# Optimization experiments

Measured on AMD Instinct MI355X. Metric: run time of the kernel, lower is better.

Reference implementation:

```python
import jax, jax.numpy as jnp
import numpy as np

B, S, D, K = 128, 200, 128, 4
NQ, NC = 10000, 500


def setup_inputs() -> dict:
    key = jax.random.key(0)
    ks = jax.random.split(key, 20)
    f = jnp.float32
    inp = {}
    inp["question_seq"] = jax.random.randint(ks[0], (B, S), 0, NQ)
    inp["hint_attempt_seq"] = jax.random.randint(ks[1], (B, S), 0, 12)
    inp["correct_seq"] = jax.random.randint(ks[2], (B, S), 0, 2)
    inp["interval_time_seq"] = jax.random.randint(ks[3], (B, S), 0, 100)
    inp["use_time_seq"] = jax.random.randint(ks[4], (B, S), 0, 100)
    inp["q2c_table"] = jax.random.randint(ks[5], (NQ, K), 0, NC)
    inp["q2c_mask_table"] = jax.random.randint(ks[6], (NQ, K), 0, 2)
    s = 0.1
    inp["embed_question"] = jax.random.normal(ks[7], (NQ, D), f) * s
    inp["embed_question_disc"] = jax.random.normal(ks[8], (NQ, 1), f) * s
    inp["embed_concept"] = jax.random.normal(ks[9], (NC, D), f) * s
    inp["embed_interval_time"] = jax.random.normal(ks[10], (100, D), f) * s
    inp["embed_use_time"] = jax.random.normal(ks[11], (100, D), f) * s
    inp["embed_hint_attempt"] = jax.random.normal(ks[12], (12, D), f) * s
    inp["W_fuse"] = jax.random.normal(ks[13], (2 * D, D), f) / np.float32(np.sqrt(2 * D))
    inp["b_fuse"] = jnp.zeros((D,), f)
    inp["W_absorb"] = jax.random.normal(ks[14], (3 * D, D), f) / np.float32(np.sqrt(3 * D))
    inp["b_absorb"] = jnp.zeros((D,), f)
    inp["W_forget"] = jax.random.normal(ks[15], (3 * D, D), f) / np.float32(np.sqrt(3 * D))
    inp["b_forget"] = jnp.zeros((D,), f)
    inp["latent0"] = jax.random.normal(ks[16], (B, D), f) * 0.1  # xavier-init latent_pre
    return inp


def _cos(a, b, eps=1e-8):
    # torch.cosine_similarity semantics with eps clamp on each norm
    num = jnp.sum(a * b, axis=-1)
    na = jnp.sqrt(jnp.sum(a * a, axis=-1))
    nb = jnp.sqrt(jnp.sum(b * b, axis=-1))
    return num / (jnp.maximum(na, eps) * jnp.maximum(nb, eps))


def _forward(question_seq, hint_attempt_seq, correct_seq, interval_time_seq, use_time_seq,
             q2c_table, q2c_mask_table,
             embed_question, embed_question_disc, embed_concept, embed_interval_time,
             embed_use_time, embed_hint_attempt,
             W_fuse, b_fuse, W_absorb, b_absorb, W_forget, b_forget, latent0):
    f = latent0.dtype
    qe = embed_question[question_seq]                                # [B,S,D]
    qd = jax.nn.sigmoid(embed_question_disc[question_seq]) * 10.0    # [B,S,1]
    ce = jnp.broadcast_to(correct_seq.astype(f)[:, :, None], qe.shape)  # [B,S,D]
    ite = embed_interval_time[interval_time_seq]                     # [B,S,D]
    ute = embed_use_time[use_time_seq]                               # [B,S,D]
    hae = embed_hint_attempt[hint_attempt_seq]                       # [B,S,D]
    cp = embed_concept[q2c_table[question_seq]]                      # [B,S,K,D]
    m = q2c_mask_table[question_seq].astype(f)                       # [B,S,K]

    tm = lambda x: jnp.swapaxes(x, 0, 1)  # time-major for scan
    xs = (tm(qe[:, :-1]), tm(ce[:, :-1]), tm(ute[:, :-1]), tm(hae[:, :-1]), tm(ite[:, :-1]),
          tm(cp[:, :-1]), tm(cp[:, 1:]), tm(qd[:, 1:]), tm(m[:, :-1]))

    def step(lp, x):
        qe_t, ce_t, ute_t, hae_t, ite_t, cp_t, cp_t1, qd_t1, m_t = x
        inter = jnp.concatenate([qe_t, ce_t], axis=-1) @ W_fuse + b_fuse
        absorb = jnp.concatenate([inter, ute_t, hae_t], axis=-1) @ W_absorb + b_absorb
        forget = jax.nn.sigmoid(jnp.concatenate([lp, ite_t, inter], axis=-1) @ W_forget + b_forget)
        lc = lp * forget + absorb  # dropout p=0 -> identity
        qdiff = (_cos(qe_t[:, None, :], cp_t) + 1.0) * 0.5   # [B,K]
        uab = (_cos(lc[:, None, :], cp_t1) + 1.0) * 0.5      # [B,K]
        logit = qd_t1[:, 0] * jnp.sum((uab - qdiff) * m_t, axis=-1)  # [B]
        return lc, jax.nn.sigmoid(logit)

    _, ys = jax.lax.scan(step, latent0, xs)  # ys: [S-1, B]
    y = jnp.concatenate([ys.T, jnp.zeros((latent0.shape[0], 1), f)], axis=1)  # [B,S], last col 0
    return y


def reference(question_seq, hint_attempt_seq, correct_seq, interval_time_seq, use_time_seq,
              q2c_table, q2c_mask_table,
              embed_question, embed_question_disc, embed_concept, embed_interval_time,
              embed_use_time, embed_hint_attempt,
              W_fuse, b_fuse, W_absorb, b_absorb, W_forget, b_forget, latent0):
    return _forward(question_seq, hint_attempt_seq, correct_seq, interval_time_seq, use_time_seq,
                    q2c_table, q2c_mask_table,
                    embed_question, embed_question_disc, embed_concept, embed_interval_time,
                    embed_use_time, embed_hint_attempt,
                    W_fuse, b_fuse, W_absorb, b_absorb, W_forget, b_forget, latent0)
```

## Files before the change

### kernel.cpp

```cpp
#include <hip/hip_runtime.h>
#include <hip/hip_bf16.h>

typedef unsigned short u16;

#define Bb  128
#define Ss  200
#define Tt  199
#define Dd  128
#define Kk  4
#define NQq 10000
#define NCc 500
#define CHK 16
#define NCH 13

__device__ inline float bf2f(u16 u) {
    union { unsigned int i; float f; } x;
    x.i = ((unsigned int)u) << 16;
    return x.f;
}

__device__ inline float ldf(const void* p, int i, int m) {
    if (m) return ((const float*)p)[i];
    return bf2f(((const u16*)p)[i]);
}

__device__ inline void stf(void* p, int i, int m, float v) {
    if (m) ((float*)p)[i] = v;
    else ((__hip_bfloat16*)p)[i] = __float2bfloat16(v);
}

__device__ inline int clampi(int v, int lo, int hi) {
    return v < lo ? lo : (v > hi ? hi : v);
}

__device__ inline float wave_red(float v) {
#pragma unroll
    for (int m = 32; m >= 1; m >>= 1) v += __shfl_xor(v, m);
    return v;
}

__device__ inline float4 f4add(float4 a, float4 b) {
    return make_float4(a.x + b.x, a.y + b.y, a.z + b.z, a.w + b.w);
}
__device__ inline float4 f4fma(float s, float4 a, float4 b) {
    return make_float4(fmaf(s, a.x, b.x), fmaf(s, a.y, b.y),
                       fmaf(s, a.z, b.z), fmaf(s, a.w, b.w));
}

__device__ inline int detect_mode(const void* Eq) {
    const u16* q = (const u16*)Eq;
    const int l = threadIdx.x & 63;
    float mx = 0.f;
#pragma unroll
    for (int k = 0; k < 4; ++k) {
        float a = fabsf(bf2f(q[l * 4 + k]));
        if (!(a == a)) a = 3.0e38f;
        mx = fmaxf(mx, a);
    }
#pragma unroll
    for (int s = 32; s >= 1; s >>= 1) mx = fmaxf(mx, __shfl_xor(mx, s));
    return (mx > 1.0e6f) ? 1 : 0;
}

__global__ __launch_bounds__(128) void k_prep(
    const void* Eq, const void* Wf, const void* Wa, const void* Wg,
    const void* bfu, const void* ba, const void* bg,
    const void* Eut, const void* Eha, const void* Eit, const void* Ec,
    float* cnorm, float* BabT, float* BfgT,
    float* vA0, float* vA1, float* vF0, float* vF1,
    float* PA_ut, float* PA_ha, float* PF_it) {
    const int m = detect_mode(Eq);
    const int bi = blockIdx.x, tid = threadIdx.x;
    __shared__ float cs2s[128];
    __shared__ float tmp[2];
    if (bi < 500) {
        const int c = bi;
        float v = ldf(Ec, c * 128 + tid, m);
        float s = wave_red(v * v);
        if ((tid & 63) == 0) tmp[tid >> 6] = s;
        __syncthreads();
        if (tid == 0) cnorm[c] = fmaxf(sqrtf(tmp[0] + tmp[1]), 1e-8f);
    } else if (bi < 628) {
        const int r = bi - 500;
        float acc = 0.f;
        for (int j = 0; j < 128; ++j)
            acc += ldf(Wf, r * 128 + j, m) * ldf(Wa, j * 128 + tid, m);
        BabT[r * 128 + tid] = acc;
    } else if (bi < 756) {
        const int r = bi - 628;
        float acc = 0.f;
        for (int j = 0; j < 128; ++j)
            acc += ldf(Wf, r * 128 + j, m) * ldf(Wg, (256 + j) * 128 + tid, m);
        BfgT[r * 128 + tid] = acc;
    } else if (bi == 756) {
        float s = 0.f;
        for (int r = 0; r < 128; ++r) s += ldf(Wf, (128 + r) * 128 + tid, m);
        cs2s[tid] = s;
        __syncthreads();
        float a0 = 0.f, a1 = 0.f;
        for (int j = 0; j < 128; ++j) {
            float wv = ldf(Wa, j * 128 + tid, m);
            a0 += ldf(bfu, j, m) * wv;
            a1 += cs2s[j] * wv;
        }
        vA0[tid] = a0 + ldf(ba, tid, m);
        vA1[tid] = a1;
    } else if (bi == 757) {
        float s = 0.f;
        for (int r = 0; r < 128; ++r) s += ldf(Wf, (128 + r) * 128 + tid, m);
        cs2s[tid] = s;
        __syncthreads();
        float a0 = 0.f, a1 = 0.f;
        for (int j = 0; j < 128; ++j) {
            float wv = ldf(Wg, (256 + j) * 128 + tid, m);
            a0 += ldf(bfu, j, m) * wv;
            a1 += cs2s[j] * wv;
        }
        vF0[tid] = a0 + ldf(bg, tid, m);
        vF1[tid] = a1;
    } else if (bi < 858) {
        const int r = bi - 758;
        float acc = 0.f;
        for (int j = 0; j < 128; ++j)
            acc += ldf(Eut, r * 128 + j, m) * ldf(Wa, (128 + j) * 128 + tid, m);
        PA_ut[r * 128 + tid] = acc;
    } else if (bi < 870) {
        const int r = bi - 858;
        float acc = 0.f;
        for (int j = 0; j < 128; ++j)
            acc += ldf(Eha, r * 128 + j, m) * ldf(Wa, (256 + j) * 128 + tid, m);
        PA_ha[r * 128 + tid] = acc;
    } else {
        const int r = bi - 870;
        float acc = 0.f;
        for (int j = 0; j < 128; ++j)
            acc += ldf(Eit, r * 128 + j, m) * ldf(Wg, (128 + j) * 128 + tid, m);
        PF_it[r * 128 + tid] = acc;
    }
}

__global__ __launch_bounds__(256) void k_mid(
    const void* Eq, const void* Eqd, const void* Ec,
    const int* q2c, const int* q2cm,
    const float* BabT, const float* BfgT, const float* cnorm,
    float* PA_q, float* PF_q, float* qdm, float* qd10) {
    const int m = detect_mode(Eq);
    const int tid = threadIdx.x;
    const int bi = blockIdx.x;
    if (bi < 313) {
        __shared__ float At[32][36];
        __shared__ float Bt0[32][128];
        __shared__ float Bt1[32][128];
        const int r0 = bi * 32;
        float acc0[2][8], acc1[2][8];
#pragma unroll
        for (int j = 0; j < 2; ++j)
#pragma unroll
            for (int i = 0; i < 8; ++i) { acc0[j][i] = 0.f; acc1[j][i] = 0.f; }
        const int tx = tid & 15, ty = tid >> 4;
        for (int ks = 0; ks < 4; ++ks) {
            {
                const int row = tid >> 3, seg = tid & 7;
                const int q = clampi(r0 + row, 0, NQq - 1);
                const int ei = q * 128 + ks * 32 + seg * 4;
                float* dst = &At[row][seg * 4];
                if (m) {
                    float4 v = *(const float4*)((const float*)Eq + ei);
                    dst[0] = v.x; dst[1] = v.y; dst[2] = v.z; dst[3] = v.w;
                } else {
                    uint2 v = *(const uint2*)((const u16*)Eq + ei);
                    dst[0] = bf2f((u16)(v.x & 0xffff)); dst[1] = bf2f((u16)(v.x >> 16));
                    dst[2] = bf2f((u16)(v.y & 0xffff)); dst[3] = bf2f((u16)(v.y >> 16));
                }
            }
            {
                const float4* s0 = (const float4*)(BabT + ks * 32 * 128);
                const float4* s1 = (const float4*)(BfgT + ks * 32 * 128);
                float4* d0 = (float4*)&Bt0[0][0];
                float4* d1 = (float4*)&Bt1[0][0];
#pragma unroll
                for (int k = 0; k < 4; ++k) {
                    d0[tid + k * 256] = s0[tid + k * 256];
                    d1[tid + k * 256] = s1[tid + k * 256];
                }
            }
            __syncthreads();
#pragma unroll
            for (int kk = 0; kk < 32; kk += 4) {
                float a_[2][4];
                *(float4*)&a_[0][0] = *(const float4*)&At[ty * 2 + 0][kk];
                *(float4*)&a_[1][0] = *(const float4*)&At[ty * 2 + 1][kk];
#pragma unroll
                for (int q = 0; q < 4; ++q) {
                    float4 b0 = *(const float4*)&Bt0[kk + q][tx * 8];
                    float4 b1 = *(const float4*)&Bt0[kk + q][tx * 8 + 4];
                    float4 c0 = *(const float4*)&Bt1[kk + q][tx * 8];
                    float4 c1 = *(const float4*)&Bt1[kk + q][tx * 8 + 4];
#pragma unroll
                    for (int j = 0; j < 2; ++j) {
                        const float av = a_[j][q];
                        acc0[j][0] += av * b0.x; acc0[j][1] += av * b0.y;
                        acc0[j][2] += av * b0.z; acc0[j][3] += av * b0.w;
                        acc0[j][4] += av * b1.x; acc0[j][5] += av * b1.y;
                        acc0[j][6] += av * b1.z; acc0[j][7] += av * b1.w;
                        acc1[j][0] += av * c0.x; acc1[j][1] += av * c0.y;
                        acc1[j][2] += av * c0.z; acc1[j][3] += av * c0.w;
                        acc1[j][4] += av * c1.x; acc1[j][5] += av * c1.y;
                        acc1[j][6] += av * c1.z; acc1[j][7] += av * c1.w;
                    }
                }
            }
            __syncthreads();
        }
#pragma unroll
        for (int j = 0; j < 2; ++j) {
            const int q = r0 + ty * 2 + j;
            if (q < NQq) {
                float* oa = PA_q + q * 128 + tx * 8;
                float* of = PF_q + q * 128 + tx * 8;
#pragma unroll
                for (int i = 0; i < 8; ++i) { oa[i] = acc0[j][i]; of[i] = acc1[j][i]; }
            }
        }
    } else {
        const int wv = tid >> 6, lane = tid & 63;
        const int q = (bi - 313) * 4 + wv;
        const float qa = ldf(Eq, q * 128 + lane, m);
        const float qb = ldf(Eq, q * 128 + 64 + lane, m);
        const float nqc = fmaxf(sqrtf(wave_red(qa * qa + qb * qb)), 1e-8f);
        const int4 cc = ((const int4*)q2c)[q];
        const int4 mm = ((const int4*)q2cm)[q];
        const int cks[4] = {clampi(cc.x, 0, NCc - 1), clampi(cc.y, 0, NCc - 1),
                            clampi(cc.z, 0, NCc - 1), clampi(cc.w, 0, NCc - 1)};
        const int ms[4]  = {mm.x, mm.y, mm.z, mm.w};
        float qs = 0.f;
#pragma unroll
        for (int k = 0; k < 4; ++k) {
            const int ck = cks[k];
            float dot = wave_red(qa * ldf(Ec, ck * 128 + lane, m) +
                                 qb * ldf(Ec, ck * 128 + 64 + lane, m));
            qs += (float)ms[k] * (0.5f * dot / (nqc * cnorm[ck]) + 0.5f);
        }
        if (lane == 0) {
            qdm[q] = qs;
            qd10[q] = 10.f / (1.f + __expf(-ldf(Eqd, q, m)));
        }
    }
}

__global__ __launch_bounds__(256) void p4_scan(
    const int* q_seq, const int* ut_seq, const int* ha_seq, const int* it_seq,
    const int* c_seq,
    const void* Eq, const void* Wg, const void* L0,
    const float* PA_q, const float* PA_ut, const float* PA_ha,
    const float* PF_q, const float* PF_it,
    const float* vA0, const float* vA1, const float* vF0, const float* vF1,
    float* lc_seq) {
    const int m = detect_mode(Eq);
    const int b = blockIdx.x;
    const int tid = threadIdx.x;
    const int wv = tid >> 6, l = tid & 63;
    const int d0 = 2 * l;
    const int ib = wv << 5;
    const int dd = ib + (l & 31);

    __shared__ float part[2][4][128];
    __shared__ float st_ab[CHK * 128];
    __shared__ float st_pf[CHK * 128];

    float wA[32], wB[32];
#pragma unroll
    for (int k = 0; k < 32; ++k) {
        wA[k] = ldf(Wg, (ib + k) * 128 + d0, m);
        wB[k] = ldf(Wg, (ib + k) * 128 + d0 + 1, m);
    }
    float lc = (l < 32) ? ldf(L0, b * 128 + dd, m) : 0.f;

    const int srow = tid >> 4, seg = tid & 15;
    const int off8 = seg * 8;
    const float4 A0a = *(const float4*)(vA0 + off8), A0b = *(const float4*)(vA0 + off8 + 4);
    const float4 A1a = *(const float4*)(vA1 + off8), A1b = *(const float4*)(vA1 + off8 + 4);
    const float4 F0a = *(const float4*)(vF0 + off8), F0b = *(const float4*)(vF0 + off8 + 4);
    const float4 F1a = *(const float4*)(vF1 + off8), F1b = *(const float4*)(vF1 + off8 + 4);

    float4 qa0, qa1, ua0, ua1, ga0, ga1, qf0, qf1, if0, if1;
    float cf;
#define LOAD_CHUNK(C)                                                          \
    {                                                                          \
        int tt = (C) * CHK + srow; if (tt > Tt - 1) tt = Tt - 1;               \
        const int base = b * Ss + tt;                                          \
        const int qt = clampi(q_seq[base], 0, NQq - 1);                        \
        const int ut = clampi(ut_seq[base], 0, 99);                            \
        const int ha = clampi(ha_seq[base], 0, 11);                            \
        const int it = clampi(it_seq[base], 0, 99);                            \
        cf = (float)c_seq[base];                                               \
        const float* pq = PA_q + qt * 128 + off8;                              \
        qa0 = *(const float4*)pq; qa1 = *(const float4*)(pq + 4);              \
        const float* pu = PA_ut + ut * 128 + off8;                             \
        ua0 = *(const float4*)pu; ua1 = *(const float4*)(pu + 4);              \
        const float* ph = PA_ha + ha * 128 + off8;                             \
        ga0 = *(const float4*)ph; ga1 = *(const float4*)(ph + 4);              \
        const float* pf = PF_q + qt * 128 + off8;                              \
        qf0 = *(const float4*)pf; qf1 = *(const float4*)(pf + 4);              \
        const float* pi = PF_it + it * 128 + off8;                             \
        if0 = *(const float4*)pi; if1 = *(const float4*)(pi + 4);              \
    }

    LOAD_CHUNK(0)
    float lcbuf[CHK];
    int par = 0;

    for (int c = 0; c < NCH; ++c) {
        __syncthreads();
        {
            float4 ab0 = f4fma(cf, A1a, f4add(f4add(qa0, ua0), f4add(ga0, A0a)));
            float4 ab1 = f4fma(cf, A1b, f4add(f4add(qa1, ua1), f4add(ga1, A0b)));
            float4 pf0 = f4fma(cf, F1a, f4add(qf0, f4add(if0, F0a)));
            float4 pf1 = f4fma(cf, F1b, f4add(qf1, f4add(if1, F0b)));
            float4* sa = (float4*)(st_ab + srow * 128 + off8);
            sa[0] = ab0; sa[1] = ab1;
            float4* sp = (float4*)(st_pf + srow * 128 + off8);
            sp[0] = pf0; sp[1] = pf1;
        }
        if (c + 1 < NCH) LOAD_CHUNK(c + 1)
        __syncthreads();

#pragma unroll
        for (int s = 0; s < CHK; ++s) {
            float pa = 0.f, pb = 0.f;
#pragma unroll
            for (int k = 0; k < 32; ++k) {
                const float u = __uint_as_float(
                    __builtin_amdgcn_readlane(__float_as_uint(lc), k));
                pa = fmaf(u, wA[k], pa);
                pb = fmaf(u, wB[k], pb);
            }
            *(float2*)&part[par][wv][d0] = make_float2(pa, pb);
            __syncthreads();
            if (l < 32) {
                const float fs = part[par][0][dd] + part[par][1][dd]
                               + part[par][2][dd] + part[par][3][dd];
                const float ab = st_ab[(s << 7) + dd];
                const float pf = st_pf[(s << 7) + dd];
                const float fg = 1.f / (1.f + __expf(-(fs + pf)));
                lc = lc * fg + ab;
                lcbuf[s] = lc;
            }
            par ^= 1;
        }
        if (l < 32) {
#pragma unroll
            for (int s = 0; s < CHK; ++s) {
                const int t = c * CHK + s;
                if (t < Tt)
                    lc_seq[((long)t * 128 + b) * 128 + dd] = lcbuf[s];
            }
        }
    }
#undef LOAD_CHUNK
}

__global__ __launch_bounds__(256) void p5_out(
    const int* q_seq, const int* q2c, const int* q2cm,
    const float* lc_seq, const float* qdm, const float* qd10,
    const float* cnorm, const void* Eq, const void* Ec, void* out) {
    const int m = detect_mode(Eq);
    const int wv = threadIdx.x >> 6, lane = threadIdx.x & 63;
    const int r = blockIdx.x * 4 + wv;
    const int t = r >> 7, b = r & 127;
    const int qt  = clampi(q_seq[b * Ss + t], 0, NQq - 1);
    const int qt1 = clampi(q_seq[b * Ss + t + 1], 0, NQq - 1);
    const int4 mm = ((const int4*)q2cm)[qt];
    int4 ci = ((const int4*)q2c)[qt1];
    const int c0 = clampi(ci.x, 0, NCc - 1), c1 = clampi(ci.y, 0, NCc - 1);
    const int c2 = clampi(ci.z, 0, NCc - 1), c3 = clampi(ci.w, 0, NCc - 1);
    const float la = lc_seq[(long)r * 128 + lane];
    const float lb = lc_seq[(long)r * 128 + 64 + lane];
    float nl = la * la + lb * lb;
    float d0 = la * ldf(Ec, c0 * 128 + lane, m) + lb * ldf(Ec, c0 * 128 + 64 + lane, m);
    float d1 = la * ldf(Ec, c1 * 128 + lane, m) + lb * ldf(Ec, c1 * 128 + 64 + lane, m);
    float d2 = la * ldf(Ec, c2 * 128 + lane, m) + lb * ldf(Ec, c2 * 128 + 64 + lane, m);
    float d3 = la * ldf(Ec, c3 * 128 + lane, m) + lb * ldf(Ec, c3 * 128 + 64 + lane, m);
#pragma unroll
    for (int s = 32; s >= 1; s >>= 1) {
        nl += __shfl_xor(nl, s);
        d0 += __shfl_xor(d0, s); d1 += __shfl_xor(d1, s);
        d2 += __shfl_xor(d2, s); d3 += __shfl_xor(d3, s);
    }
    if (lane == 0) {
        const float inl = 1.f / fmaxf(sqrtf(nl), 1e-8f);
        const float accv = (float)mm.x * (0.5f * d0 * inl / cnorm[c0] + 0.5f)
                         + (float)mm.y * (0.5f * d1 * inl / cnorm[c1] + 0.5f)
                         + (float)mm.z * (0.5f * d2 * inl / cnorm[c2] + 0.5f)
                         + (float)mm.w * (0.5f * d3 * inl / cnorm[c3] + 0.5f);
        const float logit = qd10[qt1] * (accv - qdm[qt]);
        stf(out, b * Ss + t, m, 1.f / (1.f + __expf(-logit)));
        if (t == 0) stf(out, b * Ss + 199, m, 0.f);
    }
}

extern "C" void kernel_launch(void* const* d_in, const int* in_sizes, int n_in,
                              void* d_out, int out_size, void* d_ws, size_t ws_size,
                              hipStream_t stream) {
    (void)in_sizes; (void)n_in; (void)out_size; (void)ws_size;
    const int* q_seq  = (const int*)d_in[0];
    const int* ha_seq = (const int*)d_in[1];
    const int* c_seq  = (const int*)d_in[2];
    const int* it_seq = (const int*)d_in[3];
    const int* ut_seq = (const int*)d_in[4];
    const int* q2c    = (const int*)d_in[5];
    const int* q2cm   = (const int*)d_in[6];
    const void* Eq   = d_in[7];
    const void* Eqd  = d_in[8];
    const void* Ec   = d_in[9];
    const void* Eit  = d_in[10];
    const void* Eut  = d_in[11];
    const void* Eha  = d_in[12];
    const void* Wf   = d_in[13];
    const void* bfu  = d_in[14];
    const void* Wa   = d_in[15];
    const void* ba   = d_in[16];
    const void* Wg   = d_in[17];
    const void* bg   = d_in[18];
    const void* L0   = d_in[19];

    float* cnorm = (float*)d_ws;
    float* vA0   = cnorm + 512;
    float* vA1   = vA0 + 128;
    float* vF0   = vA1 + 128;
    float* vF1   = vF0 + 128;
    float* BabT  = vF1 + 128;
    float* BfgT  = BabT + 16384;
    float* PA_ut = BfgT + 16384;
    float* PA_ha = PA_ut + 12800;
    float* PF_it = PA_ha + 1536;
    float* qdm   = PF_it + 12800;
    float* qd10  = qdm + 10016;
    float* PA_q  = qd10 + 10016;
    float* PF_q  = PA_q + 1280000;
    float* lc_seq= PF_q + 1280000;

    hipLaunchKernelGGL(k_prep, dim3(970), dim3(128), 0, stream,
                       Eq, Wf, Wa, Wg, bfu, ba, bg, Eut, Eha, Eit, Ec,
                       cnorm, BabT, BfgT, vA0, vA1, vF0, vF1, PA_ut, PA_ha, PF_it);
    hipLaunchKernelGGL(k_mid, dim3(2813), dim3(256), 0, stream,
                       Eq, Eqd, Ec, q2c, q2cm, BabT, BfgT, cnorm,
                       PA_q, PF_q, qdm, qd10);
    hipLaunchKernelGGL(p4_scan, dim3(Bb), dim3(256), 0, stream,
                       q_seq, ut_seq, ha_seq, it_seq, c_seq, Eq, Wg, L0,
                       PA_q, PA_ut, PA_ha, PF_q, PF_it,
                       vA0, vA1, vF0, vF1, lc_seq);
    hipLaunchKernelGGL(p5_out, dim3(Tt * Bb / 4), dim3(256), 0, stream,
                       q_seq, q2c, q2cm, lc_seq, qdm, qd10, cnorm, Eq, Ec, d_out);
}
```

Before: 235.4 us.

## Restructure prep kernels, inline concept norms, and overlap chunk loads in scan

Moves the question-difficulty work out of the GEMM kernel into k_prep, packs paired matmul rows into 256-thread blocks, and splits the PA_q/PF_q GEMM into its own kernel. Concept norms are now recomputed inline with a wave reduction instead of coming from a precomputed cnorm table, which removes that dependency. In the scan, the next chunk's prefetch is moved to step 1 so it overlaps compute. The absorb and forget values are preloaded into registers, and the readlane dot products use two accumulators to shorten the dependency chain. The cost is extra shuffle reductions for the norms in p5_out and the qdm jobs.

```diff
diff --git a/kernel.cpp b/kernel.cpp
--- a/kernel.cpp
+++ b/kernel.cpp
@@ -6,8 +6,6 @@
 #define Bb  128
 #define Ss  200
 #define Tt  199
-#define Dd  128
-#define Kk  4
 #define NQq 10000
 #define NCc 500
 #define CHK 16
@@ -62,169 +60,78 @@
     return (mx > 1.0e6f) ? 1 : 0;
 }
 
-__global__ __launch_bounds__(128) void k_prep(
-    const void* Eq, const void* Wf, const void* Wa, const void* Wg,
+__global__ __launch_bounds__(256) void k_prep(
+    const void* Eq, const void* Eqd, const void* Wf, const void* Wa, const void* Wg,
     const void* bfu, const void* ba, const void* bg,
     const void* Eut, const void* Eha, const void* Eit, const void* Ec,
-    float* cnorm, float* BabT, float* BfgT,
+    const int* q2c, const int* q2cm,
+    float* BabT, float* BfgT,
     float* vA0, float* vA1, float* vF0, float* vF1,
-    float* PA_ut, float* PA_ha, float* PF_it) {
+    float* PA_ut, float* PA_ha, float* PF_it, float* qdm, float* qd10) {
     const int m = detect_mode(Eq);
-    const int bi = blockIdx.x, tid = threadIdx.x;
+    const int job = blockIdx.x, tid = threadIdx.x;
     __shared__ float cs2s[128];
-    __shared__ float tmp[2];
-    if (bi < 500) {
-        const int c = bi;
-        float v = ldf(Ec, c * 128 + tid, m);
-        float s = wave_red(v * v);
-        if ((tid & 63) == 0) tmp[tid >> 6] = s;
-        __syncthreads();
-        if (tid == 0) cnorm[c] = fmaxf(sqrtf(tmp[0] + tmp[1]), 1e-8f);
-    } else if (bi < 628) {
-        const int r = bi - 500;
+    if (job < 128) {
+        const int r = job, col = tid & 127;
         float acc = 0.f;
-        for (int j = 0; j < 128; ++j)
-            acc += ldf(Wf, r * 128 + j, m) * ldf(Wa, j * 128 + tid, m);
-        BabT[r * 128 + tid] = acc;
-    } else if (bi < 756) {
-        const int r = bi - 628;
-        float acc = 0.f;
-        for (int j = 0; j < 128; ++j)
-            acc += ldf(Wf, r * 128 + j, m) * ldf(Wg, (256 + j) * 128 + tid, m);
-        BfgT[r * 128 + tid] = acc;
-    } else if (bi == 756) {
-        float s = 0.f;
-        for (int r = 0; r < 128; ++r) s += ldf(Wf, (128 + r) * 128 + tid, m);
-        cs2s[tid] = s;
+        if (tid < 128) {
+            for (int j = 0; j < 128; ++j)
+                acc += ldf(Wf, r * 128 + j, m) * ldf(Wa, j * 128 + col, m);
+            BabT[r * 128 + col] = acc;
+        } else {
+            for (int j = 0; j < 128; ++j)
+                acc += ldf(Wf, r * 128 + j, m) * ldf(Wg, (256 + j) * 128 + col, m);
+            BfgT[r * 128 + col] = acc;
+        }
+    } else if (job == 128) {
+        const int col = tid & 127;
+        if (tid < 128) {
+            float s = 0.f;
+            for (int r2 = 0; r2 < 128; ++r2) s += ldf(Wf, (128 + r2) * 128 + col, m);
+            cs2s[col] = s;
+        }
         __syncthreads();
         float a0 = 0.f, a1 = 0.f;
-        for (int j = 0; j < 128; ++j) {
-            float wv = ldf(Wa, j * 128 + tid, m);
-            a0 += ldf(bfu, j, m) * wv;
-            a1 += cs2s[j] * wv;
-        }
-        vA0[tid] = a0 + ldf(ba, tid, m);
-        vA1[tid] = a1;
-    } else if (bi == 757) {
-        float s = 0.f;
-        for (int r = 0; r < 128; ++r) s += ldf(Wf, (128 + r) * 128 + tid, m);
-        cs2s[tid] = s;
-        __syncthreads();
-        float a0 = 0.f, a1 = 0.f;
-        for (int j = 0; j < 128; ++j) {
-            float wv = ldf(Wg, (256 + j) * 128 + tid, m);
-            a0 += ldf(bfu, j, m) * wv;
-            a1 += cs2s[j] * wv;
-        }
-        vF0[tid] = a0 + ldf(bg, tid, m);
-        vF1[tid] = a1;
-    } else if (bi < 858) {
-        const int r = bi - 758;
+        if (tid < 128) {
+            for (int j = 0; j < 128; ++j) {
+                const float wv = ldf(Wa, j * 128 + col, m);
+                a0 += ldf(bfu, j, m) * wv;
+                a1 += cs2s[j] * wv;
+            }
+            vA0[col] = a0 + ldf(ba, col, m);
+            vA1[col] = a1;
+        } else {
+            for (int j = 0; j < 128; ++j) {
+                const float wv = ldf(Wg, (256 + j) * 128 + col, m);
+                a0 += ldf(bfu, j, m) * wv;
+                a1 += cs2s[j] * wv;
+            }
+            vF0[col] = a0 + ldf(bg, col, m);
+            vF1[col] = a1;
+        }
+    } else if (job < 229) {
+        const int r = job - 129, col = tid & 127;
         float acc = 0.f;
-        for (int j = 0; j < 128; ++j)
-            acc += ldf(Eut, r * 128 + j, m) * ldf(Wa, (128 + j) * 128 + tid, m);
-        PA_ut[r * 128 + tid] = acc;
-    } else if (bi < 870) {
-        const int r = bi - 858;
-        float acc = 0.f;
-        for (int j = 0; j < 128; ++j)
-            acc += ldf(Eha, r * 128 + j, m) * ldf(Wa, (256 + j) * 128 + tid, m);
-        PA_ha[r * 128 + tid] = acc;
-    } else {
-        const int r = bi - 870;
-        float acc = 0.f;
-        for (int j = 0; j < 128; ++j)
-            acc += ldf(Eit, r * 128 + j, m) * ldf(Wg, (128 + j) * 128 + tid, m);
-        PF_it[r * 128 + tid] = acc;
-    }
-}
-
-__global__ __launch_bounds__(256) void k_mid(
-    const void* Eq, const void* Eqd, const void* Ec,
-    const int* q2c, const int* q2cm,
-    const float* BabT, const float* BfgT, const float* cnorm,
-    float* PA_q, float* PF_q, float* qdm, float* qd10) {
-    const int m = detect_mode(Eq);
-    const int tid = threadIdx.x;
-    const int bi = blockIdx.x;
-    if (bi < 313) {
-        __shared__ float At[32][36];
-        __shared__ float Bt0[32][128];
-        __shared__ float Bt1[32][128];
-        const int r0 = bi * 32;
-        float acc0[2][8], acc1[2][8];
-#pragma unroll
-        for (int j = 0; j < 2; ++j)
-#pragma unroll
-            for (int i = 0; i < 8; ++i) { acc0[j][i] = 0.f; acc1[j][i] = 0.f; }
-        const int tx = tid & 15, ty = tid >> 4;
-        for (int ks = 0; ks < 4; ++ks) {
-            {
-                const int row = tid >> 3, seg = tid & 7;
-                const int q = clampi(r0 + row, 0, NQq - 1);
-                const int ei = q * 128 + ks * 32 + seg * 4;
-                float* dst = &At[row][seg * 4];
-                if (m) {
-                    float4 v = *(const float4*)((const float*)Eq + ei);
-                    dst[0] = v.x; dst[1] = v.y; dst[2] = v.z; dst[3] = v.w;
-                } else {
-                    uint2 v = *(const uint2*)((const u16*)Eq + ei);
-                    dst[0] = bf2f((u16)(v.x & 0xffff)); dst[1] = bf2f((u16)(v.x >> 16));
-                    dst[2] = bf2f((u16)(v.y & 0xffff)); dst[3] = bf2f((u16)(v.y >> 16));
-                }
-            }
-            {
-                const float4* s0 = (const float4*)(BabT + ks * 32 * 128);
-                const float4* s1 = (const float4*)(BfgT + ks * 32 * 128);
-                float4* d0 = (float4*)&Bt0[0][0];
-                float4* d1 = (float4*)&Bt1[0][0];
-#pragma unroll
-                for (int k = 0; k < 4; ++k) {
-                    d0[tid + k * 256] = s0[tid + k * 256];
-                    d1[tid + k * 256] = s1[tid + k * 256];
-                }
-            }
-            __syncthreads();
-#pragma unroll
-            for (int kk = 0; kk < 32; kk += 4) {
-                float a_[2][4];
-                *(float4*)&a_[0][0] = *(const float4*)&At[ty * 2 + 0][kk];
-                *(float4*)&a_[1][0] = *(const float4*)&At[ty * 2 + 1][kk];
-#pragma unroll
-                for (int q = 0; q < 4; ++q) {
-                    float4 b0 = *(const float4*)&Bt0[kk + q][tx * 8];
-                    float4 b1 = *(const float4*)&Bt0[kk + q][tx * 8 + 4];
-                    float4 c0 = *(const float4*)&Bt1[kk + q][tx * 8];
-                    float4 c1 = *(const float4*)&Bt1[kk + q][tx * 8 + 4];
-#pragma unroll
-                    for (int j = 0; j < 2; ++j) {
-                        const float av = a_[j][q];
-                        acc0[j][0] += av * b0.x; acc0[j][1] += av * b0.y;
-                        acc0[j][2] += av * b0.z; acc0[j][3] += av * b0.w;
-                        acc0[j][4] += av * b1.x; acc0[j][5] += av * b1.y;
-                        acc0[j][6] += av * b1.z; acc0[j][7] += av * b1.w;
-                        acc1[j][0] += av * c0.x; acc1[j][1] += av * c0.y;
-                        acc1[j][2] += av * c0.z; acc1[j][3] += av * c0.w;
-                        acc1[j][4] += av * c1.x; acc1[j][5] += av * c1.y;
-                        acc1[j][6] += av * c1.z; acc1[j][7] += av * c1.w;
-                    }
-                }
-            }
-            __syncthreads();
-        }
-#pragma unroll
-        for (int j = 0; j < 2; ++j) {
-            const int q = r0 + ty * 2 + j;
-            if (q < NQq) {
-                float* oa = PA_q + q * 128 + tx * 8;
-                float* of = PF_q + q * 128 + tx * 8;
-#pragma unroll
-                for (int i = 0; i < 8; ++i) { oa[i] = acc0[j][i]; of[i] = acc1[j][i]; }
-            }
+        if (tid < 128) {
+            for (int j = 0; j < 128; ++j)
+                acc += ldf(Eut, r * 128 + j, m) * ldf(Wa, (128 + j) * 128 + col, m);
+            PA_ut[r * 128 + col] = acc;
+        } else {
+            for (int j = 0; j < 128; ++j)
+                acc += ldf(Eit, r * 128 + j, m) * ldf(Wg, (128 + j) * 128 + col, m);
+            PF_it[r * 128 + col] = acc;
+        }
+    } else if (job < 241) {
+        const int r = job - 229;
+        if (tid < 128) {
+            float acc = 0.f;
+            for (int j = 0; j < 128; ++j)
+                acc += ldf(Eha, r * 128 + j, m) * ldf(Wa, (256 + j) * 128 + tid, m);
+            PA_ha[r * 128 + tid] = acc;
         }
     } else {
         const int wv = tid >> 6, lane = tid & 63;
-        const int q = (bi - 313) * 4 + wv;
+        const int q = (job - 241) * 4 + wv;
         const float qa = ldf(Eq, q * 128 + lane, m);
         const float qb = ldf(Eq, q * 128 + 64 + lane, m);
         const float nqc = fmaxf(sqrtf(wave_red(qa * qa + qb * qb)), 1e-8f);
@@ -237,13 +144,96 @@
 #pragma unroll
         for (int k = 0; k < 4; ++k) {
             const int ck = cks[k];
-            float dot = wave_red(qa * ldf(Ec, ck * 128 + lane, m) +
-                                 qb * ldf(Ec, ck * 128 + 64 + lane, m));
-            qs += (float)ms[k] * (0.5f * dot / (nqc * cnorm[ck]) + 0.5f);
+            const float ea = ldf(Ec, ck * 128 + lane, m);
+            const float eb = ldf(Ec, ck * 128 + 64 + lane, m);
+            const float dot = wave_red(qa * ea + qb * eb);
+            const float nn = fmaxf(sqrtf(wave_red(ea * ea + eb * eb)), 1e-8f);
+            qs += (float)ms[k] * (0.5f * dot / (nqc * nn) + 0.5f);
         }
         if (lane == 0) {
             qdm[q] = qs;
             qd10[q] = 10.f / (1.f + __expf(-ldf(Eqd, q, m)));
+        }
+    }
+}
+
+__global__ __launch_bounds__(256) void k_gemm(
+    const void* Eq, const float* BabT, const float* BfgT,
+    float* PA_q, float* PF_q) {
+    const int m = detect_mode(Eq);
+    const int tid = threadIdx.x;
+    __shared__ float At[32][36];
+    __shared__ float Bt0[32][128];
+    __shared__ float Bt1[32][128];
+    const int r0 = blockIdx.x * 32;
+    float acc0[2][8], acc1[2][8];
+#pragma unroll
+    for (int j = 0; j < 2; ++j)
+#pragma unroll
+        for (int i = 0; i < 8; ++i) { acc0[j][i] = 0.f; acc1[j][i] = 0.f; }
+    const int tx = tid & 15, ty = tid >> 4;
+    for (int ks = 0; ks < 4; ++ks) {
+        {
+            const int row = tid >> 3, seg = tid & 7;
+            const int q = clampi(r0 + row, 0, NQq - 1);
+            const int ei = q * 128 + ks * 32 + seg * 4;
+            float* dst = &At[row][seg * 4];
+            if (m) {
+                float4 v = *(const float4*)((const float*)Eq + ei);
+                dst[0] = v.x; dst[1] = v.y; dst[2] = v.z; dst[3] = v.w;
+            } else {
+                uint2 v = *(const uint2*)((const u16*)Eq + ei);
+                dst[0] = bf2f((u16)(v.x & 0xffff)); dst[1] = bf2f((u16)(v.x >> 16));
+                dst[2] = bf2f((u16)(v.y & 0xffff)); dst[3] = bf2f((u16)(v.y >> 16));
+            }
+        }
+        {
+            const float4* s0 = (const float4*)(BabT + ks * 32 * 128);
+            const float4* s1 = (const float4*)(BfgT + ks * 32 * 128);
+            float4* d0 = (float4*)&Bt0[0][0];
+            float4* d1 = (float4*)&Bt1[0][0];
+#pragma unroll
+            for (int k = 0; k < 4; ++k) {
+                d0[tid + k * 256] = s0[tid + k * 256];
+                d1[tid + k * 256] = s1[tid + k * 256];
+            }
+        }
+        __syncthreads();
+#pragma unroll
+        for (int kk = 0; kk < 32; kk += 4) {
+            float a_[2][4];
+            *(float4*)&a_[0][0] = *(const float4*)&At[ty * 2 + 0][kk];
+            *(float4*)&a_[1][0] = *(const float4*)&At[ty * 2 + 1][kk];
+#pragma unroll
+            for (int q = 0; q < 4; ++q) {
+                float4 b0 = *(const float4*)&Bt0[kk + q][tx * 8];
+                float4 b1 = *(const float4*)&Bt0[kk + q][tx * 8 + 4];
+                float4 c0 = *(const float4*)&Bt1[kk + q][tx * 8];
+                float4 c1 = *(const float4*)&Bt1[kk + q][tx * 8 + 4];
+#pragma unroll
+                for (int j = 0; j < 2; ++j) {
+                    const float av = a_[j][q];
+                    acc0[j][0] += av * b0.x; acc0[j][1] += av * b0.y;
+                    acc0[j][2] += av * b0.z; acc0[j][3] += av * b0.w;
+                    acc0[j][4] += av * b1.x; acc0[j][5] += av * b1.y;
+                    acc0[j][6] += av * b1.z; acc0[j][7] += av * b1.w;
+                    acc1[j][0] += av * c0.x; acc1[j][1] += av * c0.y;
+                    acc1[j][2] += av * c0.z; acc1[j][3] += av * c0.w;
+                    acc1[j][4] += av * c1.x; acc1[j][5] += av * c1.y;
+                    acc1[j][6] += av * c1.z; acc1[j][7] += av * c1.w;
+                }
+            }
+        }
+        __syncthreads();
+    }
+#pragma unroll
+    for (int j = 0; j < 2; ++j) {
+        const int q = r0 + ty * 2 + j;
+        if (q < NQq) {
+            float* oa = PA_q + q * 128 + tx * 8;
+            float* of = PF_q + q * 128 + tx * 8;
+#pragma unroll
+            for (int i = 0; i < 8; ++i) { oa[i] = acc0[j][i]; of[i] = acc1[j][i]; }
         }
     }
 }
@@ -322,29 +312,38 @@
             float4* sp = (float4*)(st_pf + srow * 128 + off8);
             sp[0] = pf0; sp[1] = pf1;
         }
-        if (c + 1 < NCH) LOAD_CHUNK(c + 1)
         __syncthreads();
 
+        float abr = 0.f, pfr = 0.f;
+        if (l < 32) { abr = st_ab[dd]; pfr = st_pf[dd]; }
+
 #pragma unroll
         for (int s = 0; s < CHK; ++s) {
-            float pa = 0.f, pb = 0.f;
-#pragma unroll
-            for (int k = 0; k < 32; ++k) {
-                const float u = __uint_as_float(
+            float pa0 = 0.f, pa1 = 0.f, pb0 = 0.f, pb1 = 0.f;
+#pragma unroll
+            for (int k = 0; k < 32; k += 2) {
+                const float u0 = __uint_as_float(
                     __builtin_amdgcn_readlane(__float_as_uint(lc), k));
-                pa = fmaf(u, wA[k], pa);
-                pb = fmaf(u, wB[k], pb);
-            }
-            *(float2*)&part[par][wv][d0] = make_float2(pa, pb);
+                const float u1 = __uint_as_float(
+                    __builtin_amdgcn_readlane(__float_as_uint(lc), k + 1));
+                pa0 = fmaf(u0, wA[k], pa0);
+                pb0 = fmaf(u0, wB[k], pb0);
+                pa1 = fmaf(u1, wA[k + 1], pa1);
+                pb1 = fmaf(u1, wB[k + 1], pb1);
+            }
+            *(float2*)&part[par][wv][d0] = make_float2(pa0 + pa1, pb0 + pb1);
+            if (s == 1 && c + 1 < NCH) LOAD_CHUNK(c + 1)
             __syncthreads();
             if (l < 32) {
                 const float fs = part[par][0][dd] + part[par][1][dd]
                                + part[par][2][dd] + part[par][3][dd];
-                const float ab = st_ab[(s << 7) + dd];
-                const float pf = st_pf[(s << 7) + dd];
-                const float fg = 1.f / (1.f + __expf(-(fs + pf)));
-                lc = lc * fg + ab;
+                const float fg = 1.f / (1.f + __expf(-(fs + pfr)));
+                lc = lc * fg + abr;
                 lcbuf[s] = lc;
+                if (s + 1 < CHK) {
+                    abr = st_ab[((s + 1) << 7) + dd];
+                    pfr = st_pf[((s + 1) << 7) + dd];
+                }
             }
             par ^= 1;
         }
@@ -363,7 +362,7 @@
 __global__ __launch_bounds__(256) void p5_out(
     const int* q_seq, const int* q2c, const int* q2cm,
     const float* lc_seq, const float* qdm, const float* qd10,
-    const float* cnorm, const void* Eq, const void* Ec, void* out) {
+    const void* Eq, const void* Ec, void* out) {
     const int m = detect_mode(Eq);
     const int wv = threadIdx.x >> 6, lane = threadIdx.x & 63;
     const int r = blockIdx.x * 4 + wv;
@@ -376,23 +375,30 @@
     const int c2 = clampi(ci.z, 0, NCc - 1), c3 = clampi(ci.w, 0, NCc - 1);
     const float la = lc_seq[(long)r * 128 + lane];
     const float lb = lc_seq[(long)r * 128 + 64 + lane];
+    const float e0a = ldf(Ec, c0 * 128 + lane, m), e0b = ldf(Ec, c0 * 128 + 64 + lane, m);
+    const float e1a = ldf(Ec, c1 * 128 + lane, m), e1b = ldf(Ec, c1 * 128 + 64 + lane, m);
+    const float e2a = ldf(Ec, c2 * 128 + lane, m), e2b = ldf(Ec, c2 * 128 + 64 + lane, m);
+    const float e3a = ldf(Ec, c3 * 128 + lane, m), e3b = ldf(Ec, c3 * 128 + 64 + lane, m);
     float nl = la * la + lb * lb;
-    float d0 = la * ldf(Ec, c0 * 128 + lane, m) + lb * ldf(Ec, c0 * 128 + 64 + lane, m);
-    float d1 = la * ldf(Ec, c1 * 128 + lane, m) + lb * ldf(Ec, c1 * 128 + 64 + lane, m);
-    float d2 = la * ldf(Ec, c2 * 128 + lane, m) + lb * ldf(Ec, c2 * 128 + 64 + lane, m);
-    float d3 = la * ldf(Ec, c3 * 128 + lane, m) + lb * ldf(Ec, c3 * 128 + 64 + lane, m);
+    float d0 = la * e0a + lb * e0b, n0 = e0a * e0a + e0b * e0b;
+    float d1 = la * e1a + lb * e1b, n1 = e1a * e1a + e1b * e1b;
+    float d2 = la * e2a + lb * e2b, n2 = e2a * e2a + e2b * e2b;
+    float d3 = la * e3a + lb * e3b, n3 = e3a * e3a + e3b * e3b;
 #pragma unroll
     for (int s = 32; s >= 1; s >>= 1) {
         nl += __shfl_xor(nl, s);
         d0 += __shfl_xor(d0, s); d1 += __shfl_xor(d1, s);
         d2 += __shfl_xor(d2, s); d3 += __shfl_xor(d3, s);
+        n0 += __shfl_xor(n0, s); n1 += __shfl_xor(n1, s);
+        n2 += __shfl_xor(n2, s); n3 += __shfl_xor(n3, s);
     }
     if (lane == 0) {
         const float inl = 1.f / fmaxf(sqrtf(nl), 1e-8f);
-        const float accv = (float)mm.x * (0.5f * d0 * inl / cnorm[c0] + 0.5f)
-                         + (float)mm.y * (0.5f * d1 * inl / cnorm[c1] + 0.5f)
-                         + (float)mm.z * (0.5f * d2 * inl / cnorm[c2] + 0.5f)
-                         + (float)mm.w * (0.5f * d3 * inl / cnorm[c3] + 0.5f);
+        const float accv =
+              (float)mm.x * (0.5f * d0 * inl / fmaxf(sqrtf(n0), 1e-8f) + 0.5f)
+            + (float)mm.y * (0.5f * d1 * inl / fmaxf(sqrtf(n1), 1e-8f) + 0.5f)
+            + (float)mm.z * (0.5f * d2 * inl / fmaxf(sqrtf(n2), 1e-8f) + 0.5f)
+            + (float)mm.w * (0.5f * d3 * inl / fmaxf(sqrtf(n3), 1e-8f) + 0.5f);
         const float logit = qd10[qt1] * (accv - qdm[qt]);
         stf(out, b * Ss + t, m, 1.f / (1.f + __expf(-logit)));
         if (t == 0) stf(out, b * Ss + 199, m, 0.f);
@@ -424,8 +430,8 @@
     const void* bg   = d_in[18];
     const void* L0   = d_in[19];
 
-    float* cnorm = (float*)d_ws;
-    float* vA0   = cnorm + 512;
+    float* ws    = (float*)d_ws;
+    float* vA0   = ws;
     float* vA1   = vA0 + 128;
     float* vF0   = vA1 + 128;
     float* vF1   = vF0 + 128;
@@ -440,16 +446,16 @@
     float* PF_q  = PA_q + 1280000;
     float* lc_seq= PF_q + 1280000;
 
-    hipLaunchKernelGGL(k_prep, dim3(970), dim3(128), 0, stream,
-                       Eq, Wf, Wa, Wg, bfu, ba, bg, Eut, Eha, Eit, Ec,
-                       cnorm, BabT, BfgT, vA0, vA1, vF0, vF1, PA_ut, PA_ha, PF_it);
-    hipLaunchKernelGGL(k_mid, dim3(2813), dim3(256), 0, stream,
-                       Eq, Eqd, Ec, q2c, q2cm, BabT, BfgT, cnorm,
-                       PA_q, PF_q, qdm, qd10);
+    hipLaunchKernelGGL(k_prep, dim3(2741), dim3(256), 0, stream,
+                       Eq, Eqd, Wf, Wa, Wg, bfu, ba, bg, Eut, Eha, Eit, Ec,
+                       q2c, q2cm, BabT, BfgT, vA0, vA1, vF0, vF1,
+                       PA_ut, PA_ha, PF_it, qdm, qd10);
+    hipLaunchKernelGGL(k_gemm, dim3(313), dim3(256), 0, stream,
+                       Eq, BabT, BfgT, PA_q, PF_q);
     hipLaunchKernelGGL(p4_scan, dim3(Bb), dim3(256), 0, stream,
                        q_seq, ut_seq, ha_seq, it_seq, c_seq, Eq, Wg, L0,
                        PA_q, PA_ut, PA_ha, PF_q, PF_it,
                        vA0, vA1, vF0, vF1, lc_seq);
     hipLaunchKernelGGL(p5_out, dim3(Tt * Bb / 4), dim3(256), 0, stream,
-                       q_seq, q2c, q2cm, lc_seq, qdm, qd10, cnorm, Eq, Ec, d_out);
-}
+                       q_seq, q2c, q2cm, lc_seq, qdm, qd10, Eq, Ec, d_out);
+}
```

Measured after the change: 247.0 us. 1.05x slower.
